# Kernel tuning notes

Hardware: AMD Instinct MI355X
Metric: run time of the kernel (lower is better)

The kernel has to match this reference:

```python
import jax, jax.numpy as jnp
import numpy as np

N, E, IN_CH, H, C = 50000, 800000, 256, 4, 64


def setup_inputs() -> dict:
    key = jax.random.key(0)
    k1, k2, k3, k4 = jax.random.split(key, 4)
    x = jax.random.normal(k1, (N, IN_CH), dtype=jnp.float32)
    edge_index = jax.random.randint(k2, (2, E), 0, N, dtype=jnp.int64)
    W = jax.random.normal(k3, (H * C, IN_CH), dtype=jnp.float32) * 0.05
    att = jax.random.normal(k4, (H, 2 * C), dtype=jnp.float32) * 0.05
    return {"x": x, "edge_index": edge_index, "W": W, "att": att}


def reference(x, edge_index, W, att):
    n = x.shape[0]
    src, dst = edge_index[0], edge_index[1]
    # Wh: [N, H, C]
    Wh = (x @ W.T).reshape(n, H, C)
    # per-edge attention logits: [E, H]
    e_src = jnp.einsum('ehc,hc->eh', Wh[src], att[:, :C])
    e_dst = jnp.einsum('ehc,hc->eh', Wh[dst], att[:, C:])
    e = jax.nn.leaky_relu(e_src + e_dst, negative_slope=0.2)
    # segment softmax over incoming edges of each dst node
    e_max = jax.ops.segment_max(e, dst, num_segments=n)  # [N, H]
    e_exp = jnp.exp(e - e_max[dst])
    denom = jax.ops.segment_sum(e_exp, dst, num_segments=n)  # [N, H]
    alpha = e_exp / (denom[dst] + 1e-16)  # [E, H]
    # weighted aggregation: [N, H, C]
    agg = jax.ops.segment_sum(alpha[:, :, None] * Wh[src], dst, num_segments=n)
    return jax.nn.elu(agg.reshape(n, H * C))
```

## Files before the change

### kernel.cpp

```cpp
#include <hip/hip_runtime.h>
#include <hip/hip_bf16.h>
#include <cstdint>

#define HH 4
#define CC 64
#define KDIM 256
#define NOUT 256
#define BM 64
#define BK 64
#define CAP 96

typedef __attribute__((ext_vector_type(8))) short bf16x8;
typedef __attribute__((ext_vector_type(4))) float f32x4;
typedef unsigned short ushort_t;

__device__ __forceinline__ unsigned short f2bf(float f) {
  unsigned u = __float_as_uint(f);
  unsigned r = (u + 0x7fff + ((u >> 16) & 1)) >> 16;
  return (unsigned short)r;
}
__device__ __forceinline__ unsigned pk2bf(float lo, float hi) {
  return (unsigned)f2bf(lo) | ((unsigned)f2bf(hi) << 16);
}

__global__ __launch_bounds__(256)
void scatter_convW(const float* __restrict__ W, ushort_t* __restrict__ Wb,
                   const int* __restrict__ ei, int* __restrict__ cnt,
                   int* __restrict__ bucket, int wblocks, int E) {
  if ((int)blockIdx.x < wblocks) {
    int i = ((int)blockIdx.x * 256 + threadIdx.x) * 8;
    float4 a = *(const float4*)(W + i);
    float4 b = *(const float4*)(W + i + 4);
    uint4 o;
    o.x = pk2bf(a.x, a.y); o.y = pk2bf(a.z, a.w);
    o.z = pk2bf(b.x, b.y); o.w = pk2bf(b.z, b.w);
    *(uint4*)(Wb + i) = o;
  } else {
    int t = ((int)blockIdx.x - wblocks) * 256 + threadIdx.x;
    if (t < E) {
      int s = ei[t];
      int d = ei[E + t];
      int pos = atomicAdd(&cnt[d], 1);
      if (pos < CAP) bucket[(size_t)d * CAP + pos] = s;
    }
  }
}

#define GLOAD_LDS16(g, l) \
  __builtin_amdgcn_global_load_lds((__attribute__((address_space(1))) const void*)(g), \
                                   (__attribute__((address_space(3))) void*)(l), 16, 0, 0)

__global__ __launch_bounds__(256)
void gemm_direct(const float* __restrict__ X, const ushort_t* __restrict__ Wb,
                 ushort_t* __restrict__ Wh, float* __restrict__ s_src,
                 float* __restrict__ s_dst, const float* __restrict__ att, int M) {
  __shared__ char As[BM * BK * 2];
  __shared__ char Bs[NOUT * BK * 2];
  const int tid = threadIdx.x;
  const int lane = tid & 63;
  const int w = tid >> 6;
  const int row0 = blockIdx.x * BM;

  const int arow = tid >> 2;
  const int akoff = (tid & 3) * 16;
  const bool aval = (row0 + arow) < M;

  f32x4 acc[4][4] = {};

  for (int k0 = 0; k0 < KDIM; k0 += BK) {
    {
      const float* gx = X + (size_t)(row0 + arow) * KDIM + k0 + akoff;
      float4 f[4];
#pragma unroll
      for (int i = 0; i < 4; ++i)
        f[i] = aval ? *(const float4*)(gx + i * 4) : make_float4(0.f, 0.f, 0.f, 0.f);
#pragma unroll
      for (int hfl = 0; hfl < 2; ++hfl) {
        uint4 o;
        o.x = pk2bf(f[2 * hfl].x, f[2 * hfl].y);
        o.y = pk2bf(f[2 * hfl].z, f[2 * hfl].w);
        o.z = pk2bf(f[2 * hfl + 1].x, f[2 * hfl + 1].y);
        o.w = pk2bf(f[2 * hfl + 1].z, f[2 * hfl + 1].w);
        int q = (tid & 3) * 2 + hfl;
        int phys = q ^ (arow & 7);
        *(uint4*)(As + (arow * 8 + phys) * 16) = o;
      }
    }
#pragma unroll
    for (int i = 0; i < 8; ++i) {
      int c = i * 256 + tid;
      int row = c >> 3, q = (c & 7) ^ (row & 7);
      const ushort_t* gptr = Wb + (size_t)row * KDIM + k0 + q * 8;
      GLOAD_LDS16(gptr, Bs + c * 16);
    }
    __syncthreads();

#pragma unroll
    for (int kk = 0; kk < 2; ++kk) {
      bf16x8 aF[4], bF[4];
      int qq = kk * 4 + (lane >> 4);
#pragma unroll
      for (int rt = 0; rt < 4; ++rt) {
        int r = rt * 16 + (lane & 15);
        int phys = qq ^ (r & 7);
        aF[rt] = *(const bf16x8*)(As + r * 128 + phys * 16);
      }
#pragma unroll
      for (int ct = 0; ct < 4; ++ct) {
        int cl = w * 64 + ct * 16 + (lane & 15);
        int phys = qq ^ (cl & 7);
        bF[ct] = *(const bf16x8*)(Bs + cl * 128 + phys * 16);
      }
#pragma unroll
      for (int rt = 0; rt < 4; ++rt)
#pragma unroll
        for (int ct = 0; ct < 4; ++ct)
          acc[rt][ct] = __builtin_amdgcn_mfma_f32_16x16x32_bf16(aF[rt], bF[ct], acc[rt][ct], 0, 0, 0);
    }
    __syncthreads();
  }

  const int h = w;
  float att_s[4], att_d[4];
#pragma unroll
  for (int ct = 0; ct < 4; ++ct) {
    att_s[ct] = att[h * 2 * CC + ct * 16 + (lane & 15)];
    att_d[ct] = att[h * 2 * CC + CC + ct * 16 + (lane & 15)];
  }
#pragma unroll
  for (int rt = 0; rt < 4; ++rt) {
#pragma unroll
    for (int reg = 0; reg < 4; ++reg) {
      float ls = 0.f, ld_ = 0.f;
#pragma unroll
      for (int ct = 0; ct < 4; ++ct) {
        float a = acc[rt][ct][reg];
        ls += a * att_s[ct];
        ld_ += a * att_d[ct];
      }
#pragma unroll
      for (int off = 1; off < 16; off <<= 1) {
        ls += __shfl_xor(ls, off);
        ld_ += __shfl_xor(ld_, off);
      }
      int r = row0 + rt * 16 + (lane >> 4) * 4 + reg;
      if ((lane & 15) == 0 && r < M) {
        s_src[r * HH + h] = ls;
        s_dst[r * HH + h] = ld_;
      }
    }
  }

#pragma unroll
  for (int rt = 0; rt < 4; ++rt) {
#pragma unroll
    for (int reg = 0; reg < 4; ++reg) {
      int r = row0 + rt * 16 + (lane >> 4) * 4 + reg;
      if (r < M) {
#pragma unroll
        for (int ct = 0; ct < 4; ++ct) {
          int ccol = w * 64 + ct * 16 + (lane & 15);
          Wh[(size_t)r * NOUT + ccol] = f2bf(acc[rt][ct][reg]);
        }
      }
    }
  }
}

__global__ __launch_bounds__(256)
void aggregate(const ushort_t* __restrict__ Wh, const float* __restrict__ s_src,
               const float* __restrict__ s_dst, const int* __restrict__ cnt,
               const int* __restrict__ bucket, float* __restrict__ out, int N) {
  int wid = (int)((blockIdx.x * 256 + threadIdx.x) >> 6);
  int lane = threadIdx.x & 63;
  if (wid >= N) return;
  int half = lane >> 5, cl = lane & 31;
  int h = cl >> 3;
  int deg = cnt[wid];
  if (deg > CAP) deg = CAP;
  int start = wid * CAP;
  int end = start + deg;
  float sd = s_dst[wid * HH + h];
  float acc[8] = {};
  float dsum = 0.f;
  int idx = start + half;
  for (; idx + 6 < end; idx += 8) {
    int s[4];
#pragma unroll
    for (int k = 0; k < 4; ++k) s[k] = bucket[idx + 2 * k];
    float p[4];
    uint4 wv[4];
#pragma unroll
    for (int k = 0; k < 4; ++k) {
      float v = s_src[s[k] * HH + h] + sd;
      v = v > 0.f ? v : 0.2f * v;
      p[k] = __expf(v);
      wv[k] = *(const uint4*)(Wh + (size_t)s[k] * NOUT + cl * 8);
    }
#pragma unroll
    for (int k = 0; k < 4; ++k) {
      dsum += p[k];
#pragma unroll
      for (int j = 0; j < 4; ++j) {
        unsigned u = ((const unsigned*)&wv[k])[j];
        acc[2 * j]     += p[k] * __uint_as_float(u << 16);
        acc[2 * j + 1] += p[k] * __uint_as_float(u & 0xffff0000u);
      }
    }
  }
  for (; idx < end; idx += 2) {
    int s0 = bucket[idx];
    float v = s_src[s0 * HH + h] + sd;
    v = v > 0.f ? v : 0.2f * v;
    float p0 = __expf(v);
    uint4 w0 = *(const uint4*)(Wh + (size_t)s0 * NOUT + cl * 8);
    dsum += p0;
#pragma unroll
    for (int j = 0; j < 4; ++j) {
      unsigned u0 = ((const unsigned*)&w0)[j];
      acc[2 * j]     += p0 * __uint_as_float(u0 << 16);
      acc[2 * j + 1] += p0 * __uint_as_float(u0 & 0xffff0000u);
    }
  }
#pragma unroll
  for (int j = 0; j < 8; ++j) acc[j] += __shfl_xor(acc[j], 32);
  dsum += __shfl_xor(dsum, 32);
  if (half == 0) {
    float rd = 1.0f / (dsum + 1e-16f);
    float o[8];
#pragma unroll
    for (int j = 0; j < 8; ++j) {
      float a = acc[j] * rd;
      o[j] = a > 0.f ? a : expm1f(a);
    }
    float* op = out + (size_t)wid * NOUT + cl * 8;
    *(float4*)op = make_float4(o[0], o[1], o[2], o[3]);
    *(float4*)(op + 4) = make_float4(o[4], o[5], o[6], o[7]);
  }
}

extern "C" void kernel_launch(void* const* d_in, const int* in_sizes, int n_in,
                              void* d_out, int out_size, void* d_ws, size_t ws_size,
                              hipStream_t stream) {
  const float* x = (const float*)d_in[0];
  const int* ei = (const int*)d_in[1];
  const float* W = (const float*)d_in[2];
  const float* att = (const float*)d_in[3];
  float* out = (float*)d_out;
  const int N = in_sizes[0] / KDIM;
  const int E = in_sizes[1] / 2;
  const int NPAD = ((N + BM - 1) / BM) * BM;

  char* p = (char*)d_ws;
  auto alloc = [&](size_t bytes) {
    char* r = p;
    p += (bytes + 255) & ~(size_t)255;
    return r;
  };
  ushort_t* Wb   = (ushort_t*)alloc((size_t)NOUT * KDIM * 2);
  ushort_t* Wh   = (ushort_t*)alloc((size_t)NPAD * NOUT * 2);
  float* s_src   = (float*)alloc((size_t)N * HH * 4);
  float* s_dst   = (float*)alloc((size_t)N * HH * 4);
  int* cnt       = (int*)alloc((size_t)N * 4);
  int* bucket    = (int*)alloc((size_t)N * CAP * 4);

  (void)hipMemsetAsync(cnt, 0, (size_t)N * 4, stream);

  const int wblocks = (NOUT * KDIM) / (256 * 8);
  int eblocks = (E + 255) / 256;
  scatter_convW<<<wblocks + eblocks, 256, 0, stream>>>(W, Wb, ei, cnt, bucket, wblocks, E);

  gemm_direct<<<NPAD / BM, 256, 0, stream>>>(x, Wb, Wh, s_src, s_dst, att, N);

  aggregate<<<(N + 3) / 4, 256, 0, stream>>>(Wh, s_src, s_dst, cnt, bucket, out, N);
}
```

Before: 152.6 us.

## Prefetch next X tile into registers during GEMM and use nontemporal bucket stores

The GEMM K-loop is fully unrolled, and the next K-step's fp32 X loads are issued before the barrier. Explicit vmcnt waits and raw s_barriers let those loads stay in flight during the current step's MFMA work, replacing full __syncthreads. Out-of-range rows are clamped to a valid row and zeroed in registers, so the loads stay unconditional. The edge scatter also writes bucket entries with nontemporal stores to reduce cache pollution. The hand-written waitcnt counts are fragile and depend on the compiler's ordering of loads.

```diff
diff --git a/kernel.cpp b/kernel.cpp
--- a/kernel.cpp
+++ b/kernel.cpp
@@ -41,7 +41,8 @@
       int s = ei[t];
       int d = ei[E + t];
       int pos = atomicAdd(&cnt[d], 1);
-      if (pos < CAP) bucket[(size_t)d * CAP + pos] = s;
+      if (pos < CAP)
+        __builtin_nontemporal_store(s, &bucket[(size_t)d * CAP + pos]);
     }
   }
 }
@@ -64,27 +65,37 @@
   const int arow = tid >> 2;
   const int akoff = (tid & 3) * 16;
   const bool aval = (row0 + arow) < M;
+  const int arow_c = aval ? (row0 + arow) : (M - 1);
+  const float* gx_base = X + (size_t)arow_c * KDIM + akoff;
 
   f32x4 acc[4][4] = {};
-
-  for (int k0 = 0; k0 < KDIM; k0 += BK) {
+  float4 f[4];
+
+#define LOADA(k0_)                                                  \
+  {                                                                 \
+    _Pragma("unroll")                                               \
+    for (int i_ = 0; i_ < 4; ++i_)                                  \
+      f[i_] = *(const float4*)(gx_base + (k0_) + i_ * 4);           \
+  }
+
+  LOADA(0);
+
+#pragma unroll
+  for (int k = 0; k < 4; ++k) {
+    const int k0 = k * BK;
     {
-      const float* gx = X + (size_t)(row0 + arow) * KDIM + k0 + akoff;
-      float4 f[4];
-#pragma unroll
-      for (int i = 0; i < 4; ++i)
-        f[i] = aval ? *(const float4*)(gx + i * 4) : make_float4(0.f, 0.f, 0.f, 0.f);
-#pragma unroll
-      for (int hfl = 0; hfl < 2; ++hfl) {
-        uint4 o;
-        o.x = pk2bf(f[2 * hfl].x, f[2 * hfl].y);
-        o.y = pk2bf(f[2 * hfl].z, f[2 * hfl].w);
-        o.z = pk2bf(f[2 * hfl + 1].x, f[2 * hfl + 1].y);
-        o.w = pk2bf(f[2 * hfl + 1].z, f[2 * hfl + 1].w);
-        int q = (tid & 3) * 2 + hfl;
-        int phys = q ^ (arow & 7);
-        *(uint4*)(As + (arow * 8 + phys) * 16) = o;
-      }
+      float4 g0 = aval ? f[0] : make_float4(0.f, 0.f, 0.f, 0.f);
+      float4 g1 = aval ? f[1] : make_float4(0.f, 0.f, 0.f, 0.f);
+      float4 g2 = aval ? f[2] : make_float4(0.f, 0.f, 0.f, 0.f);
+      float4 g3 = aval ? f[3] : make_float4(0.f, 0.f, 0.f, 0.f);
+      uint4 o0, o1;
+      o0.x = pk2bf(g0.x, g0.y); o0.y = pk2bf(g0.z, g0.w);
+      o0.z = pk2bf(g1.x, g1.y); o0.w = pk2bf(g1.z, g1.w);
+      o1.x = pk2bf(g2.x, g2.y); o1.y = pk2bf(g2.z, g2.w);
+      o1.z = pk2bf(g3.x, g3.y); o1.w = pk2bf(g3.z, g3.w);
+      int q0 = (tid & 3) * 2;
+      *(uint4*)(As + (arow * 8 + (q0 ^ (arow & 7))) * 16) = o0;
+      *(uint4*)(As + (arow * 8 + ((q0 + 1) ^ (arow & 7))) * 16) = o1;
     }
 #pragma unroll
     for (int i = 0; i < 8; ++i) {
@@ -93,7 +104,15 @@
       const ushort_t* gptr = Wb + (size_t)row * KDIM + k0 + q * 8;
       GLOAD_LDS16(gptr, Bs + c * 16);
     }
-    __syncthreads();
+    if (k < 3) LOADA((k + 1) * BK);
+    if (k < 3) {
+      asm volatile("s_waitcnt vmcnt(4) lgkmcnt(0)" ::: "memory");
+    } else {
+      asm volatile("s_waitcnt vmcnt(0) lgkmcnt(0)" ::: "memory");
+    }
+    __builtin_amdgcn_sched_barrier(0);
+    __builtin_amdgcn_s_barrier();
+    asm volatile("" ::: "memory");
 
 #pragma unroll
     for (int kk = 0; kk < 2; ++kk) {
@@ -117,7 +136,11 @@
         for (int ct = 0; ct < 4; ++ct)
           acc[rt][ct] = __builtin_amdgcn_mfma_f32_16x16x32_bf16(aF[rt], bF[ct], acc[rt][ct], 0, 0, 0);
     }
-    __syncthreads();
+    if (k < 3) {
+      asm volatile("" ::: "memory");
+      __builtin_amdgcn_s_barrier();
+      __builtin_amdgcn_sched_barrier(0);
+    }
   }
 
   const int h = w;
```

After: 159.4 us. +4.4%, slower.

## Fold W bf16 conversion and count zeroing into GEMM, drop memset

Applied to the files above, without the earlier changes.

Removes the separate hipMemsetAsync and the W-to-bf16 conversion pass. The GEMM now zeroes the count array and converts fp32 W to bf16 itself while staging it into LDS, and the edge scatter moves to its own kernel after the GEMM. This cuts one launch plus the memset, but every GEMM block now reads fp32 W (twice the bytes) and converts it through registers instead of using direct global-to-LDS loads.

```diff
diff --git a/kernel.cpp b/kernel.cpp
--- a/kernel.cpp
+++ b/kernel.cpp
@@ -24,42 +24,33 @@
 }
 
 __global__ __launch_bounds__(256)
-void scatter_convW(const float* __restrict__ W, ushort_t* __restrict__ Wb,
-                   const int* __restrict__ ei, int* __restrict__ cnt,
-                   int* __restrict__ bucket, int wblocks, int E) {
-  if ((int)blockIdx.x < wblocks) {
-    int i = ((int)blockIdx.x * 256 + threadIdx.x) * 8;
-    float4 a = *(const float4*)(W + i);
-    float4 b = *(const float4*)(W + i + 4);
-    uint4 o;
-    o.x = pk2bf(a.x, a.y); o.y = pk2bf(a.z, a.w);
-    o.z = pk2bf(b.x, b.y); o.w = pk2bf(b.z, b.w);
-    *(uint4*)(Wb + i) = o;
-  } else {
-    int t = ((int)blockIdx.x - wblocks) * 256 + threadIdx.x;
-    if (t < E) {
-      int s = ei[t];
-      int d = ei[E + t];
-      int pos = atomicAdd(&cnt[d], 1);
-      if (pos < CAP) bucket[(size_t)d * CAP + pos] = s;
-    }
-  }
-}
-
-#define GLOAD_LDS16(g, l) \
-  __builtin_amdgcn_global_load_lds((__attribute__((address_space(1))) const void*)(g), \
-                                   (__attribute__((address_space(3))) void*)(l), 16, 0, 0)
+void scatter_k(const int* __restrict__ ei, int* __restrict__ cnt,
+               int* __restrict__ bucket, int E) {
+  int t = (int)blockIdx.x * 256 + threadIdx.x;
+  if (t < E) {
+    int s = ei[t];
+    int d = ei[E + t];
+    int pos = atomicAdd(&cnt[d], 1);
+    if (pos < CAP) bucket[(size_t)d * CAP + pos] = s;
+  }
+}
 
 __global__ __launch_bounds__(256)
-void gemm_direct(const float* __restrict__ X, const ushort_t* __restrict__ Wb,
+void gemm_direct(const float* __restrict__ X, const float* __restrict__ W,
                  ushort_t* __restrict__ Wh, float* __restrict__ s_src,
-                 float* __restrict__ s_dst, const float* __restrict__ att, int M) {
+                 float* __restrict__ s_dst, const float* __restrict__ att,
+                 int M, int* __restrict__ cnt, int N) {
   __shared__ char As[BM * BK * 2];
   __shared__ char Bs[NOUT * BK * 2];
   const int tid = threadIdx.x;
   const int lane = tid & 63;
   const int w = tid >> 6;
   const int row0 = blockIdx.x * BM;
+
+  if (tid < 64) {
+    int i = (int)blockIdx.x * 64 + tid;
+    if (i < N) cnt[i] = 0;
+  }
 
   const int arow = tid >> 2;
   const int akoff = (tid & 3) * 16;
@@ -89,9 +80,15 @@
 #pragma unroll
     for (int i = 0; i < 8; ++i) {
       int c = i * 256 + tid;
-      int row = c >> 3, q = (c & 7) ^ (row & 7);
-      const ushort_t* gptr = Wb + (size_t)row * KDIM + k0 + q * 8;
-      GLOAD_LDS16(gptr, Bs + c * 16);
+      int row = c >> 3, q = c & 7;
+      const float* gw = W + (size_t)row * KDIM + k0 + q * 8;
+      float4 g0 = *(const float4*)gw;
+      float4 g1 = *(const float4*)(gw + 4);
+      uint4 o;
+      o.x = pk2bf(g0.x, g0.y); o.y = pk2bf(g0.z, g0.w);
+      o.z = pk2bf(g1.x, g1.y); o.w = pk2bf(g1.z, g1.w);
+      int phys = q ^ (row & 7);
+      *(uint4*)(Bs + (row * 8 + phys) * 16) = o;
     }
     __syncthreads();
 
@@ -257,20 +254,15 @@
     p += (bytes + 255) & ~(size_t)255;
     return r;
   };
-  ushort_t* Wb   = (ushort_t*)alloc((size_t)NOUT * KDIM * 2);
   ushort_t* Wh   = (ushort_t*)alloc((size_t)NPAD * NOUT * 2);
   float* s_src   = (float*)alloc((size_t)N * HH * 4);
   float* s_dst   = (float*)alloc((size_t)N * HH * 4);
   int* cnt       = (int*)alloc((size_t)N * 4);
   int* bucket    = (int*)alloc((size_t)N * CAP * 4);
 
-  (void)hipMemsetAsync(cnt, 0, (size_t)N * 4, stream);
-
-  const int wblocks = (NOUT * KDIM) / (256 * 8);
-  int eblocks = (E + 255) / 256;
-  scatter_convW<<<wblocks + eblocks, 256, 0, stream>>>(W, Wb, ei, cnt, bucket, wblocks, E);
-
-  gemm_direct<<<NPAD / BM, 256, 0, stream>>>(x, Wb, Wh, s_src, s_dst, att, N);
+  gemm_direct<<<NPAD / BM, 256, 0, stream>>>(x, W, Wh, s_src, s_dst, att, N, cnt, N);
+
+  scatter_k<<<(E + 255) / 256, 256, 0, stream>>>(ei, cnt, bucket, E);
 
   aggregate<<<(N + 3) / 4, 256, 0, stream>>>(Wh, s_src, s_dst, cnt, bucket, out, N);
 }
```

Measured after the change: 151.6 us. About the same (-0.7%).
